# Performance work log

Hardware: AMD Instinct MI355X
Metric: run time of the kernel (lower is better)

Reference implementation:

```python
import jax, jax.numpy as jnp
import numpy as np

B, N, DEG = 64, 512, 16        # graphs, nodes per graph, avg degree
C, HID = 10, 128               # input feat dim (== num_classes quirk), hidden
E = B * N * DEG                # total edges (fixed; pooling masks edges)


def _gcn(x, W, b, src, dst, emask, n):
    # PyG GCNConv: add self-loops, symmetric norm D^-1/2 (A+I) D^-1/2 (XW) + b
    h = x @ W
    deg = jax.ops.segment_sum(emask, dst, num_segments=n) + 1.0  # +1 self-loop
    dinv = jax.lax.rsqrt(deg)
    norm = dinv[src] * dinv[dst] * emask
    agg = jax.ops.segment_sum(h[src] * norm[:, None], dst, num_segments=n)
    return agg + h * (dinv * dinv)[:, None] + b  # self-loop term + bias


def _sag_pool(x, src, dst, emask, Wp, bp, n_per):
    # SAGPooling: score = tanh(GCN(x)); per-graph top-k (ratio=0.5); x' = x[perm]*score
    n = x.shape[0]
    score = jnp.tanh(_gcn(x, Wp, bp, src, dst, emask, n)[:, 0])
    k = n_per // 2
    vals, idx = jax.lax.top_k(score.reshape(B, n_per), k)  # [B,k]
    perm = (idx + (jnp.arange(B) * n_per)[:, None]).reshape(-1)
    xk = x[perm] * vals.reshape(-1)[:, None]
    # relabel edges; drop edges touching removed nodes via mask (fixed E)
    mapping = jnp.full((n,), -1, jnp.int32).at[perm].set(
        jnp.arange(B * k, dtype=jnp.int32))
    ns, nd = mapping[src], mapping[dst]
    nmask = emask * ((ns >= 0) & (nd >= 0)).astype(emask.dtype)
    return xk, jnp.maximum(ns, 0), jnp.maximum(nd, 0), nmask, k


def _readout(x, k):
    # global max pool || global mean pool (all kept nodes are real, no padding)
    xg = x.reshape(B, k, -1)
    return jnp.concatenate([xg.max(axis=1), xg.mean(axis=1)], axis=1)


def setup_inputs() -> dict:
    key = jax.random.key(0)
    ks = jax.random.split(key, 16)
    x = jax.random.normal(ks[0], (B * N, C), jnp.float32)
    off = jnp.repeat(jnp.arange(B, dtype=jnp.int32) * N, N * DEG)
    src = jax.random.randint(ks[1], (E,), 0, N, jnp.int32) + off
    dst = jax.random.randint(ks[2], (E,), 0, N, jnp.int32) + off
    p = lambda k, s: jax.random.normal(k, s, jnp.float32) * 0.05
    return {
        "x": x, "src": src, "dst": dst,
        "W1": p(ks[3], (C, HID)), "b1": jnp.zeros((HID,), jnp.float32),
        "W2": p(ks[4], (HID, HID)), "b2": jnp.zeros((HID,), jnp.float32),
        "W3": p(ks[5], (HID, HID)), "b3": jnp.zeros((HID,), jnp.float32),
        "Wp": p(ks[6], (HID, 1)), "bp": jnp.zeros((1,), jnp.float32),
        "L1W": p(ks[7], (2 * HID, HID)), "L1b": jnp.zeros((HID,), jnp.float32),
        "L2W": p(ks[8], (HID, HID // 2)), "L2b": jnp.zeros((HID // 2,), jnp.float32),
    }


def reference(x, src, dst, W1, b1, W2, b2, W3, b3, Wp, bp, L1W, L1b, L2W, L2b):
    emask = jnp.ones((E,), jnp.float32)
    h = jax.nn.relu(_gcn(x, W1, b1, src, dst, emask, B * N))
    h, src, dst, emask, k = _sag_pool(h, src, dst, emask, Wp, bp, N)
    x1 = _readout(h, k)
    h = jax.nn.relu(_gcn(h, W2, b2, src, dst, emask, B * k))
    h, src, dst, emask, k = _sag_pool(h, src, dst, emask, Wp, bp, k)
    x2 = _readout(h, k)
    h = jax.nn.relu(_gcn(h, W3, b3, src, dst, emask, B * k))
    h, src, dst, emask, k = _sag_pool(h, src, dst, emask, Wp, bp, k)
    x3 = _readout(h, k)
    z = x1 + x2 + x3
    z = jax.nn.relu(z @ L1W + L1b)
    # dropout inactive in eval mode
    z = jax.nn.relu(z @ L2W + L2b)
    return jax.nn.log_softmax(z, axis=1)
```

## Files before the change

kernel.cpp:

```cpp
#include <hip/hip_runtime.h>
#include <math.h>

#define BGR 64
#define N0 512
#define NDEG 16
#define E_TOT (BGR*N0*NDEG)
#define EPG (N0*NDEG)
#define EIT (EPG/512)
#define HID 128


__global__ __launch_bounds__(512) void k_topo0(
    const int* __restrict__ s0, const int* __restrict__ d0,
    int2* __restrict__ edges, int* __restrict__ cnt, int* __restrict__ rowptr,
    float* __restrict__ dinv, int2* __restrict__ csr, float* __restrict__ z){
  __shared__ int   deg[512];
  __shared__ int   sb[512];
  __shared__ int   cur[512];
  __shared__ float dl[512];
  int g = (blockIdx.x & 7)*8 + (blockIdx.x >> 3);
  int t = threadIdx.x;
  int gbase = g*N0, ebase = g*EPG;
  deg[t] = 0;
  if (t < 256) z[g*256 + t] = 0.f;
  __syncthreads();
  int2 ebuf[EIT];
  #pragma unroll
  for (int it = 0; it < EIT; it++){
    int i = ebase + it*512 + t;
    int2 e = make_int2(s0[i], d0[i]);
    ebuf[it] = e;
    edges[i] = e;
    atomicAdd(&deg[e.y - gbase], 1);
  }
  __syncthreads();
  int vdeg = deg[t];
  sb[t] = vdeg; __syncthreads();
  for (int off = 1; off < 512; off <<= 1){
    int add = (t >= off) ? sb[t-off] : 0;
    __syncthreads(); sb[t] += add; __syncthreads();
  }
  int excl = sb[t] - vdeg;
  rowptr[gbase + t] = ebase + excl;
  cnt[gbase + t] = vdeg;
  cur[t] = excl;
  float dv = rsqrtf((float)vdeg + 1.f);
  dl[t] = dv;
  dinv[gbase + t] = dv;
  __syncthreads();
  #pragma unroll
  for (int it = 0; it < EIT; it++){
    int2 e = ebuf[it];
    int sl = e.x - gbase, dc = e.y - gbase;
    int pos = atomicAdd(&cur[dc], 1);
    csr[ebase + pos] = make_int2(e.x, __float_as_int(dl[sl]*dl[dc]));
  }
}

__global__ __launch_bounds__(512) void k_l1_fused(
    const float* __restrict__ x, const float* __restrict__ W1,
    const int2* __restrict__ csr, const int* __restrict__ rowptr,
    const int* __restrict__ cnt, const float* __restrict__ dinv,
    const float* __restrict__ b1, const float* __restrict__ Wp,
    float4* __restrict__ gout4, float* __restrict__ hp_part){
  extern __shared__ float hl[];
  int b = blockIdx.x;
  int xcd = b & 7, idx = b >> 3;
  int graph = xcd*8 + (idx >> 2);
  int qf = idx & 3;
  int t = threadIdx.x;
  int gbase = graph*N0;
  int fp = t & 31;
  int f = qf*32 + fp;
  float wcol[10];
  #pragma unroll
  for (int k = 0; k < 10; k++) wcol[k] = W1[k*HID + f];
  for (int n = t >> 5; n < N0; n += 16){
    const float* xr = x + (gbase + n)*10;
    float acc = 0.f;
    #pragma unroll
    for (int k = 0; k < 10; k++) acc += xr[k]*wcol[k];
    hl[n*32 + fp] = acc;
  }
  __syncthreads();
  const float4* hl4 = (const float4*)hl;
  int l = t & 7, grp = t >> 3;
  float4 bb = ((const float4*)b1)[qf*8 + l];
  float4 wp = ((const float4*)Wp)[qf*8 + l];
  for (int nl = grp; nl < N0; nl += 64){
    int node = gbase + nl;
    int start = rowptr[node], c = cnt[node];
    float4 acc = make_float4(0.f,0.f,0.f,0.f);
    for (int j = 0; j < c; j++){
      int2 e = csr[start + j];
      float wgt = __int_as_float(e.y);
      float4 hv = hl4[(e.x - gbase)*8 + l];
      acc.x += wgt*hv.x; acc.y += wgt*hv.y; acc.z += wgt*hv.z; acc.w += wgt*hv.w;
    }
    float di = dinv[node], dd = di*di;
    float4 hs = hl4[nl*8 + l];
    float4 v;
    v.x = fmaxf(acc.x + hs.x*dd + bb.x, 0.f);
    v.y = fmaxf(acc.y + hs.y*dd + bb.y, 0.f);
    v.z = fmaxf(acc.z + hs.z*dd + bb.z, 0.f);
    v.w = fmaxf(acc.w + hs.w*dd + bb.w, 0.f);
    gout4[node*32 + qf*8 + l] = v;
    float contrib = v.x*wp.x + v.y*wp.y + v.z*wp.z + v.w*wp.w;
    #pragma unroll
    for (int off = 4; off; off >>= 1) contrib += __shfl_down(contrib, off, 8);
    if (l == 0) hp_part[qf*32768 + node] = contrib;
  }
}

__global__ void k_gemm8(const float* __restrict__ x, const float* __restrict__ W,
                        float* __restrict__ out, int fin, int nper){
  __shared__ float xr[8][HID];
  int b = blockIdx.x;
  int xcd = b & 7, idx = b >> 3, bpg = nper >> 3;
  int graph = xcd*8 + idx / bpg;
  int base = graph*nper + (idx % bpg)*8;
  int f = threadIdx.x;
  #pragma unroll
  for (int nd = 0; nd < 8; nd++) if (f < fin) xr[nd][f] = x[(base+nd)*fin + f];
  __syncthreads();
  float acc[8] = {0,0,0,0,0,0,0,0};
  for (int i = 0; i < fin; i++){
    float wv = W[i*HID + f];
    #pragma unroll
    for (int nd = 0; nd < 8; nd++) acc[nd] += xr[nd][i]*wv;
  }
  #pragma unroll
  for (int nd = 0; nd < 8; nd++) out[(base+nd)*HID + f] = acc[nd];
}

__global__ __launch_bounds__(256) void k_gcn_gather(
    const float4* __restrict__ h4, const int2* __restrict__ csr,
    const int* __restrict__ rowptr, const int* __restrict__ cnt,
    const float* __restrict__ dinv, const float4* __restrict__ bias4,
    const float4* __restrict__ Wp4, float4* __restrict__ out4,
    float* __restrict__ hp, int nper){
  int b = blockIdx.x;
  int xcd = b & 7, idx = b >> 3, bpg = nper >> 3;
  int graph = xcd*8 + idx / bpg;
  int node = graph*nper + (idx % bpg)*8 + (threadIdx.x >> 5);
  int l = threadIdx.x & 31;
  int start = rowptr[node], c = cnt[node];
  float4 acc = make_float4(0.f, 0.f, 0.f, 0.f);
  for (int j = 0; j < c; j++){
    int2 e = csr[start + j];
    float wgt = __int_as_float(e.y);
    float4 hv = h4[e.x*32 + l];
    acc.x += wgt*hv.x; acc.y += wgt*hv.y; acc.z += wgt*hv.z; acc.w += wgt*hv.w;
  }
  float di = dinv[node], dd = di*di;
  float4 hs = h4[node*32 + l];
  float4 bb = bias4[l];
  float4 v;
  v.x = fmaxf(acc.x + hs.x*dd + bb.x, 0.f);
  v.y = fmaxf(acc.y + hs.y*dd + bb.y, 0.f);
  v.z = fmaxf(acc.z + hs.z*dd + bb.z, 0.f);
  v.w = fmaxf(acc.w + hs.w*dd + bb.w, 0.f);
  out4[node*32 + l] = v;
  float4 wp = Wp4[l];
  float contrib = v.x*wp.x + v.y*wp.y + v.z*wp.z + v.w*wp.w;
  #pragma unroll
  for (int off = 16; off; off >>= 1) contrib += __shfl_down(contrib, off, 32);
  if (l == 0) hp[node] = contrib;
}

__global__ __launch_bounds__(512) void k_mega(
    const float4* __restrict__ gout4, const float* __restrict__ hp,
    const float* __restrict__ hp_part, int l1flag,
    int2* __restrict__ csr, int* __restrict__ rowptr, int* __restrict__ cnt,
    float* __restrict__ dinv, const float* __restrict__ bp,
    int2* __restrict__ edges, float4* __restrict__ xpool4,
    float* __restrict__ z, int nper, int lastlev,
    const float* __restrict__ L1W, const float* __restrict__ L1b,
    const float* __restrict__ L2W, const float* __restrict__ L2b,
    float* __restrict__ out){
  __shared__ float sv[512];
  __shared__ int   si[512];
  __shared__ float hpl[512];
  __shared__ int   map[512];
  __shared__ int   sb[512];
  __shared__ int   cur[256];
  __shared__ float dl[256];
  __shared__ float4 pmx[16][32];
  __shared__ float4 psm[16][32];
  __shared__ float zr[256];
  __shared__ float h1[128];
  __shared__ float h2[64];
  __shared__ float red[2];
  int g = (blockIdx.x & 7)*8 + (blockIdx.x >> 3);
  int t = threadIdx.x;
  int k = nper >> 1;
  int gbase = g*nper, ebase = g*EPG, gb2 = g*k;
  bool act = t < nper;
  if (act){
    int node = gbase + t;
    hpl[t] = l1flag ? (hp_part[node] + hp_part[32768 + node] +
                       hp_part[65536 + node] + hp_part[98304 + node])
                    : hp[node];
  }
  __syncthreads();
  float v = 0.f; int idx = t;
  if (act){
    int start = rowptr[gbase + t], c = cnt[gbase + t];
    float a = 0.f;
    for (int j = 0; j < c; j++){
      int2 e = csr[start + j];
      a += __int_as_float(e.y) * hpl[e.x - gbase];
    }
    float di = dinv[gbase + t];
    v = tanhf(a + hpl[t]*di*di + bp[0]);
  }
  for (int kk = 2; kk <= nper; kk <<= 1){
    for (int jj = kk >> 1; jj > 0; jj >>= 1){
      if (jj >= 64){
        if (act){ sv[t] = v; si[t] = idx; }
        __syncthreads();
        if (act){
          int p = t ^ jj;
          float pv = sv[p]; int pi = si[p];
          bool amLower = (t & jj) == 0;
          bool dirDesc = (t & kk) == 0;
          bool betterMine = (v > pv) || (v == pv && idx < pi);
          if ((amLower == dirDesc) != betterMine){ v = pv; idx = pi; }
        }
        __syncthreads();
      } else if (act){
        float pv = __shfl_xor(v, jj);
        int   pi = __shfl_xor(idx, jj);
        bool amLower = (t & jj) == 0;
        bool dirDesc = (t & kk) == 0;
        bool betterMine = (v > pv) || (v == pv && idx < pi);
        if ((amLower == dirDesc) != betterMine){ v = pv; idx = pi; }
      }
    }
  }
  if (act){ sv[t] = v; si[t] = idx; }
  __syncthreads();
  int l = t & 31, j0 = t >> 5;
  float4 mx = make_float4(-INFINITY,-INFINITY,-INFINITY,-INFINITY);
  float4 sm = make_float4(0.f,0.f,0.f,0.f);
  for (int j = j0; j < k; j += 16){
    float val = sv[j]; int row = si[j];
    float4 hv = gout4[(gbase + row)*32 + l];
    float4 o = make_float4(hv.x*val, hv.y*val, hv.z*val, hv.w*val);
    xpool4[(gb2 + j)*32 + l] = o;
    mx.x = fmaxf(mx.x, o.x); mx.y = fmaxf(mx.y, o.y);
    mx.z = fmaxf(mx.z, o.z); mx.w = fmaxf(mx.w, o.w);
    sm.x += o.x; sm.y += o.y; sm.z += o.z; sm.w += o.w;
  }
  pmx[j0][l] = mx; psm[j0][l] = sm;
  __syncthreads();
  if (t < 32){
    float4 M = pmx[0][t], S = psm[0][t];
    #pragma unroll
    for (int q = 1; q < 16; q++){
      float4 m2 = pmx[q][t], s2 = psm[q][t];
      M.x = fmaxf(M.x, m2.x); M.y = fmaxf(M.y, m2.y);
      M.z = fmaxf(M.z, m2.z); M.w = fmaxf(M.w, m2.w);
      S.x += s2.x; S.y += s2.y; S.z += s2.z; S.w += s2.w;
    }
    float ki = 1.f/(float)k;
    float* zp = z + g*256;
    if (!lastlev){
      zp[t*4+0] += M.x; zp[t*4+1] += M.y; zp[t*4+2] += M.z; zp[t*4+3] += M.w;
      zp[128+t*4+0] += S.x*ki; zp[128+t*4+1] += S.y*ki;
      zp[128+t*4+2] += S.z*ki; zp[128+t*4+3] += S.w*ki;
    } else {
      zr[t*4+0] = zp[t*4+0] + M.x; zr[t*4+1] = zp[t*4+1] + M.y;
      zr[t*4+2] = zp[t*4+2] + M.z; zr[t*4+3] = zp[t*4+3] + M.w;
      zr[128+t*4+0] = zp[128+t*4+0] + S.x*ki;
      zr[128+t*4+1] = zp[128+t*4+1] + S.y*ki;
      zr[128+t*4+2] = zp[128+t*4+2] + S.z*ki;
      zr[128+t*4+3] = zp[128+t*4+3] + S.w*ki;
    }
  }
  if (lastlev){
    __syncthreads();
    if (t < 128){
      float a = L1b[t];
      for (int i = 0; i < 256; i++) a += zr[i]*L1W[i*128 + t];
      h1[t] = fmaxf(a, 0.f);
    }
    __syncthreads();
    if (t < 64){
      float a = L2b[t];
      for (int i = 0; i < 128; i++) a += h1[i]*L2W[i*64 + t];
      h2[t] = fmaxf(a, 0.f);
    }
    __syncthreads();
    if (t == 0){
      float mxv = -INFINITY;
      for (int i = 0; i < 64; i++) mxv = fmaxf(mxv, h2[i]);
      float s = 0.f;
      for (int i = 0; i < 64; i++) s += expf(h2[i] - mxv);
      red[0] = mxv; red[1] = logf(s);
    }
    __syncthreads();
    if (t < 64) out[g*64 + t] = h2[t] - red[0] - red[1];
    return;
  }
  if (act) map[t] = -1;
  if (t < k) sb[t] = 0;
  __syncthreads();
  if (t < k) map[si[t]] = t;
  __syncthreads();
  int2 ebuf[EIT];
  #pragma unroll
  for (int it = 0; it < EIT; it++){
    int i = ebase + it*512 + t;
    int2 e = edges[i];
    int2 ne = make_int2(-1, 0);
    if (e.x >= 0){
      int ns = map[e.x - gbase], nd = map[e.y - gbase];
      if (ns >= 0 && nd >= 0){
        ne = make_int2(gb2 + ns, gb2 + nd);
        atomicAdd(&sb[nd], 1);
      }
    }
    ebuf[it] = ne;
    edges[i] = ne;
  }
  __syncthreads();
  int vdeg = (t < k) ? sb[t] : 0;
  for (int off = 1; off < k; off <<= 1){
    int add = (t >= off && t < k) ? sb[t-off] : 0;
    __syncthreads();
    if (t < k) sb[t] += add;
    __syncthreads();
  }
  if (t < k){
    int excl = sb[t] - vdeg;
    rowptr[gb2 + t] = ebase + excl;
    cnt[gb2 + t] = vdeg;
    cur[t] = excl;
    float dv = rsqrtf((float)vdeg + 1.f);
    dl[t] = dv;
    dinv[gb2 + t] = dv;
  }
  __syncthreads();
  #pragma unroll
  for (int it = 0; it < EIT; it++){
    int2 e = ebuf[it];
    if (e.x >= 0){
      int sl = e.x - gb2, dc = e.y - gb2;
      int pos = atomicAdd(&cur[dc], 1);
      csr[ebase + pos] = make_int2(e.x, __float_as_int(dl[sl]*dl[dc]));
    }
  }
}

extern "C" void kernel_launch(void* const* d_in, const int* in_sizes, int n_in,
                              void* d_out, int out_size, void* d_ws, size_t ws_size,
                              hipStream_t stream){
  (void)in_sizes; (void)n_in; (void)out_size; (void)ws_size;
  const float* x0  = (const float*)d_in[0];
  const int*   s0  = (const int*)  d_in[1];
  const int*   d0  = (const int*)  d_in[2];
  const float* W1  = (const float*)d_in[3];  const float* b1 = (const float*)d_in[4];
  const float* W2  = (const float*)d_in[5];  const float* b2 = (const float*)d_in[6];
  const float* W3  = (const float*)d_in[7];  const float* b3 = (const float*)d_in[8];
  const float* Wp  = (const float*)d_in[9];  const float* bp = (const float*)d_in[10];
  const float* L1W = (const float*)d_in[11]; const float* L1b = (const float*)d_in[12];
  const float* L2W = (const float*)d_in[13]; const float* L2b = (const float*)d_in[14];
  float* out = (float*)d_out;

  float* w = (float*)d_ws;
  float* h     = w; w += 32768*HID;
  float* gout  = w; w += 32768*HID;
  float* xpA   = h    + 16384*HID;
  float* xpB   = gout + 16384*HID;
  float* xpC   = xpA;
  float* dinvv = w; w += 32768;
  float* hp    = w; w += 32768;
  float* hppt  = w; w += 4*32768;
  float* z     = w; w += BGR*256;
  int* cnt     = (int*)w; w += 32768;
  int* rowptr  = (int*)w; w += 32768;
  int2* edges  = (int2*)w; w += E_TOT*2;
  int2* csr    = (int2*)w; w += E_TOT*2;

  k_topo0<<<BGR, 512, 0, stream>>>(s0, d0, edges, cnt, rowptr, dinvv, csr, z);

  k_l1_fused<<<256, 512, 65536, stream>>>(x0, W1, csr, rowptr, cnt, dinvv,
                                          b1, Wp, (float4*)gout, hppt);
  k_mega<<<BGR, 512, 0, stream>>>((const float4*)gout, hp, hppt, 1, csr, rowptr,
                                  cnt, dinvv, bp, edges, (float4*)xpA, z, 512, 0,
                                  L1W, L1b, L2W, L2b, out);
  k_gemm8<<<16384/8, HID, 0, stream>>>(xpA, W2, h, HID, 256);
  k_gcn_gather<<<16384/8, 256, 0, stream>>>((const float4*)h, csr, rowptr, cnt, dinvv,
                                            (const float4*)b2, (const float4*)Wp,
                                            (float4*)gout, hp, 256);
  k_mega<<<BGR, 512, 0, stream>>>((const float4*)gout, hp, hppt, 0, csr, rowptr,
                                  cnt, dinvv, bp, edges, (float4*)xpB, z, 256, 0,
                                  L1W, L1b, L2W, L2b, out);
  k_gemm8<<<8192/8, HID, 0, stream>>>(xpB, W3, h, HID, 128);
  k_gcn_gather<<<8192/8, 256, 0, stream>>>((const float4*)h, csr, rowptr, cnt, dinvv,
                                           (const float4*)b3, (const float4*)Wp,
                                           (float4*)gout, hp, 128);
  k_mega<<<BGR, 512, 0, stream>>>((const float4*)gout, hp, hppt, 0, csr, rowptr,
                                  cnt, dinvv, bp, edges, (float4*)xpC, z, 128, 1,
                                  L1W, L1b, L2W, L2b, out);
}
```

Before: 254.5 us.

## Unroll CSR gathers by four, widen gemm to 16 rows, skip final pooled write

The edge-gather loops in the layer-1 fused kernel, the GCN gather kernel and the score aggregation in k_mega are unrolled by four, so several independent loads are in flight at once. The node-feature GEMM now handles 16 nodes per block instead of 8, which halves how often each W column is loaded and hardcodes the input width to HID. The last pooling level no longer writes pooled features that nothing reads. In exchange the gemm uses more registers and can launch fewer blocks, and the reassociated sums change floating-point rounding slightly.

After: 248.4 us. 2.4% less time.

```diff
diff --git a/kernel.cpp b/kernel.cpp
--- a/kernel.cpp
+++ b/kernel.cpp
@@ -3,10 +3,9 @@
 
 #define BGR 64
 #define N0 512
-#define NDEG 16
-#define E_TOT (BGR*N0*NDEG)
-#define EPG (N0*NDEG)
-#define EIT (EPG/512)
+#define E_TOT (BGR*N0*16)
+#define EPG 8192
+#define EIT 16
 #define HID 128
 
 
@@ -91,7 +90,22 @@
     int node = gbase + nl;
     int start = rowptr[node], c = cnt[node];
     float4 acc = make_float4(0.f,0.f,0.f,0.f);
-    for (int j = 0; j < c; j++){
+    int j = 0;
+    for (; j + 4 <= c; j += 4){
+      int2 e0 = csr[start+j],   e1 = csr[start+j+1];
+      int2 e2 = csr[start+j+2], e3 = csr[start+j+3];
+      float4 h0 = hl4[(e0.x - gbase)*8 + l];
+      float4 h1 = hl4[(e1.x - gbase)*8 + l];
+      float4 h2 = hl4[(e2.x - gbase)*8 + l];
+      float4 h3 = hl4[(e3.x - gbase)*8 + l];
+      float w0 = __int_as_float(e0.y), w1 = __int_as_float(e1.y);
+      float w2 = __int_as_float(e2.y), w3 = __int_as_float(e3.y);
+      acc.x += w0*h0.x + w1*h1.x + w2*h2.x + w3*h3.x;
+      acc.y += w0*h0.y + w1*h1.y + w2*h2.y + w3*h3.y;
+      acc.z += w0*h0.z + w1*h1.z + w2*h2.z + w3*h3.z;
+      acc.w += w0*h0.w + w1*h1.w + w2*h2.w + w3*h3.w;
+    }
+    for (; j < c; j++){
       int2 e = csr[start + j];
       float wgt = __int_as_float(e.y);
       float4 hv = hl4[(e.x - gbase)*8 + l];
@@ -112,25 +126,27 @@
   }
 }
 
-__global__ void k_gemm8(const float* __restrict__ x, const float* __restrict__ W,
-                        float* __restrict__ out, int fin, int nper){
-  __shared__ float xr[8][HID];
+__global__ void k_gemm16(const float* __restrict__ x, const float* __restrict__ W,
+                         float* __restrict__ out, int nper){
+  __shared__ float xr[16][HID];
   int b = blockIdx.x;
-  int xcd = b & 7, idx = b >> 3, bpg = nper >> 3;
+  int xcd = b & 7, idx = b >> 3, bpg = nper >> 4;
   int graph = xcd*8 + idx / bpg;
-  int base = graph*nper + (idx % bpg)*8;
+  int base = graph*nper + (idx % bpg)*16;
   int f = threadIdx.x;
   #pragma unroll
-  for (int nd = 0; nd < 8; nd++) if (f < fin) xr[nd][f] = x[(base+nd)*fin + f];
-  __syncthreads();
-  float acc[8] = {0,0,0,0,0,0,0,0};
-  for (int i = 0; i < fin; i++){
+  for (int nd = 0; nd < 16; nd++) xr[nd][f] = x[(base+nd)*HID + f];
+  __syncthreads();
+  float acc[16];
+  #pragma unroll
+  for (int nd = 0; nd < 16; nd++) acc[nd] = 0.f;
+  for (int i = 0; i < HID; i++){
     float wv = W[i*HID + f];
     #pragma unroll
-    for (int nd = 0; nd < 8; nd++) acc[nd] += xr[nd][i]*wv;
-  }
-  #pragma unroll
-  for (int nd = 0; nd < 8; nd++) out[(base+nd)*HID + f] = acc[nd];
+    for (int nd = 0; nd < 16; nd++) acc[nd] += xr[nd][i]*wv;
+  }
+  #pragma unroll
+  for (int nd = 0; nd < 16; nd++) out[(base+nd)*HID + f] = acc[nd];
 }
 
 __global__ __launch_bounds__(256) void k_gcn_gather(
@@ -146,7 +162,22 @@
   int l = threadIdx.x & 31;
   int start = rowptr[node], c = cnt[node];
   float4 acc = make_float4(0.f, 0.f, 0.f, 0.f);
-  for (int j = 0; j < c; j++){
+  int j = 0;
+  for (; j + 4 <= c; j += 4){
+    int2 e0 = csr[start+j],   e1 = csr[start+j+1];
+    int2 e2 = csr[start+j+2], e3 = csr[start+j+3];
+    float4 h0 = h4[e0.x*32 + l];
+    float4 h1 = h4[e1.x*32 + l];
+    float4 h2 = h4[e2.x*32 + l];
+    float4 h3 = h4[e3.x*32 + l];
+    float w0 = __int_as_float(e0.y), w1 = __int_as_float(e1.y);
+    float w2 = __int_as_float(e2.y), w3 = __int_as_float(e3.y);
+    acc.x += w0*h0.x + w1*h1.x + w2*h2.x + w3*h3.x;
+    acc.y += w0*h0.y + w1*h1.y + w2*h2.y + w3*h3.y;
+    acc.z += w0*h0.z + w1*h1.z + w2*h2.z + w3*h3.z;
+    acc.w += w0*h0.w + w1*h1.w + w2*h2.w + w3*h3.w;
+  }
+  for (; j < c; j++){
     int2 e = csr[start + j];
     float wgt = __int_as_float(e.y);
     float4 hv = h4[e.x*32 + l];
@@ -169,8 +200,8 @@
 }
 
 __global__ __launch_bounds__(512) void k_mega(
-    const float4* __restrict__ gout4, const float* __restrict__ hp,
-    const float* __restrict__ hp_part, int l1flag,
+    const float4* __restrict__ gout4, const float* __restrict__ hp_part,
+    int l1flag, const float* __restrict__ hp,
     int2* __restrict__ csr, int* __restrict__ rowptr, int* __restrict__ cnt,
     float* __restrict__ dinv, const float* __restrict__ bp,
     int2* __restrict__ edges, float4* __restrict__ xpool4,
@@ -207,9 +238,18 @@
   if (act){
     int start = rowptr[gbase + t], c = cnt[gbase + t];
     float a = 0.f;
-    for (int j = 0; j < c; j++){
+    int j = 0;
+    for (; j + 4 <= c; j += 4){
+      int2 e0 = csr[start+j],   e1 = csr[start+j+1];
+      int2 e2 = csr[start+j+2], e3 = csr[start+j+3];
+      a += __int_as_float(e0.y)*hpl[e0.x - gbase]
+         + __int_as_float(e1.y)*hpl[e1.x - gbase]
+         + __int_as_float(e2.y)*hpl[e2.x - gbase]
+         + __int_as_float(e3.y)*hpl[e3.x - gbase];
+    }
+    for (; j < c; j++){
       int2 e = csr[start + j];
-      a += __int_as_float(e.y) * hpl[e.x - gbase];
+      a += __int_as_float(e.y)*hpl[e.x - gbase];
     }
     float di = dinv[gbase + t];
     v = tanhf(a + hpl[t]*di*di + bp[0]);
@@ -247,7 +287,7 @@
     float val = sv[j]; int row = si[j];
     float4 hv = gout4[(gbase + row)*32 + l];
     float4 o = make_float4(hv.x*val, hv.y*val, hv.z*val, hv.w*val);
-    xpool4[(gb2 + j)*32 + l] = o;
+    if (!lastlev) xpool4[(gb2 + j)*32 + l] = o;
     mx.x = fmaxf(mx.x, o.x); mx.y = fmaxf(mx.y, o.y);
     mx.z = fmaxf(mx.z, o.z); mx.w = fmaxf(mx.w, o.w);
     sm.x += o.x; sm.y += o.y; sm.z += o.z; sm.w += o.w;
@@ -380,28 +420,30 @@
   float* z     = w; w += BGR*256;
   int* cnt     = (int*)w; w += 32768;
   int* rowptr  = (int*)w; w += 32768;
-  int2* edges  = (int2*)w; w += E_TOT*2;
-  int2* csr    = (int2*)w; w += E_TOT*2;
+  int2* edges  = (int2*)w; w += 2*E_TOT;
+  int2* csr    = (int2*)w; w += 2*E_TOT;
 
   k_topo0<<<BGR, 512, 0, stream>>>(s0, d0, edges, cnt, rowptr, dinvv, csr, z);
 
   k_l1_fused<<<256, 512, 65536, stream>>>(x0, W1, csr, rowptr, cnt, dinvv,
                                           b1, Wp, (float4*)gout, hppt);
-  k_mega<<<BGR, 512, 0, stream>>>((const float4*)gout, hp, hppt, 1, csr, rowptr,
+  k_mega<<<BGR, 512, 0, stream>>>((const float4*)gout, hppt, 1, hp, csr, rowptr,
                                   cnt, dinvv, bp, edges, (float4*)xpA, z, 512, 0,
                                   L1W, L1b, L2W, L2b, out);
-  k_gemm8<<<16384/8, HID, 0, stream>>>(xpA, W2, h, HID, 256);
-  k_gcn_gather<<<16384/8, 256, 0, stream>>>((const float4*)h, csr, rowptr, cnt, dinvv,
-                                            (const float4*)b2, (const float4*)Wp,
-                                            (float4*)gout, hp, 256);
-  k_mega<<<BGR, 512, 0, stream>>>((const float4*)gout, hp, hppt, 0, csr, rowptr,
+  k_gemm16<<<16384/16, HID, 0, stream>>>(xpA, W2, h, 256);
+  k_gcn_gather<<<16384/8, 256, 0, stream>>>((const float4*)h, csr, rowptr, cnt,
+                                            dinvv, (const float4*)b2,
+                                            (const float4*)Wp, (float4*)gout,
+                                            hp, 256);
+  k_mega<<<BGR, 512, 0, stream>>>((const float4*)gout, hppt, 0, hp, csr, rowptr,
                                   cnt, dinvv, bp, edges, (float4*)xpB, z, 256, 0,
                                   L1W, L1b, L2W, L2b, out);
-  k_gemm8<<<8192/8, HID, 0, stream>>>(xpB, W3, h, HID, 128);
-  k_gcn_gather<<<8192/8, 256, 0, stream>>>((const float4*)h, csr, rowptr, cnt, dinvv,
-                                           (const float4*)b3, (const float4*)Wp,
-                                           (float4*)gout, hp, 128);
-  k_mega<<<BGR, 512, 0, stream>>>((const float4*)gout, hp, hppt, 0, csr, rowptr,
+  k_gemm16<<<8192/16, HID, 0, stream>>>(xpB, W3, h, 128);
+  k_gcn_gather<<<8192/8, 256, 0, stream>>>((const float4*)h, csr, rowptr, cnt,
+                                           dinvv, (const float4*)b3,
+                                           (const float4*)Wp, (float4*)gout,
+                                           hp, 128);
+  k_mega<<<BGR, 512, 0, stream>>>((const float4*)gout, hppt, 0, hp, csr, rowptr,
                                   cnt, dinvv, bp, edges, (float4*)xpC, z, 128, 1,
                                   L1W, L1b, L2W, L2b, out);
 }
```
